# Kernel optimization log

Hardware: AMD Instinct MI355X
Metric: run time of the kernel (lower is better)

The kernel has to match this reference:

```python
import jax, jax.numpy as jnp
import numpy as np

OUT, IN = 4096, 4096
NNZ = 838860  # 0.05 * OUT * IN
ALPHA = 1.0   # set_privacy(True)


def setup_inputs() -> dict:
    key = jax.random.key(0)
    k1, k2, k3, k4, k5, k6 = jax.random.split(key, 6)
    x = jax.random.normal(k1, (2, 2048, IN), dtype=jnp.float32)
    # packed uint4 pairs stored as bytes (kept in int32 per spec; values in [0,256))
    base_packed = jax.random.randint(k2, (OUT, IN // 2), 0, 256, dtype=jnp.int32)
    # per-row dequant scales (positive, small, like ceiling/7)
    scales = jax.random.uniform(k3, (OUT, 1), dtype=jnp.float32, minval=1e-3, maxval=5e-2)
    ortho_vals = jax.random.normal(k4, (NNZ,), dtype=jnp.float32) * 0.02
    ortho_rows = jax.random.randint(k5, (NNZ,), 0, OUT, dtype=jnp.int32)
    ortho_cols = jax.random.randint(k6, (NNZ,), 0, IN, dtype=jnp.int32)
    return {"x": x, "base_packed": base_packed, "scales": scales,
            "ortho_vals": ortho_vals, "ortho_rows": ortho_rows, "ortho_cols": ortho_cols}


def _dequant(base_packed, scales):
    # unpack two int4 values per byte: col 2k <- low nibble, col 2k+1 <- high nibble
    p = base_packed.astype(jnp.int32)
    low = p & 0xF
    high = (p >> 4) & 0xF
    O, K = p.shape
    w_int4 = jnp.stack([low, high], axis=-1).reshape(O, 2 * K) - 8  # offset-binary -> [-8, 7]
    return w_int4.astype(jnp.float32) * scales  # [O, I]


def reference(x, base_packed, scales, ortho_vals, ortho_rows, ortho_cols):
    O = base_packed.shape[0]
    I = 2 * base_packed.shape[1]
    w_base = _dequant(base_packed, scales)  # [O, I] fp32
    # sparse outlier residual scattered into dense weight (CSR spmm equivalent)
    w_corr = jnp.zeros((O, I), jnp.float32).at[ortho_rows, ortho_cols].add(ortho_vals)
    w = w_base + ALPHA * w_corr
    x_flat = x.reshape(-1, I).astype(jnp.float32)
    out = x_flat @ w.T  # [N, O]
    return out.reshape(x.shape[:-1] + (O,)).astype(x.dtype)
```

## Files before the change

### kernel.cpp

```cpp
#include <hip/hip_runtime.h>
#include <cstdint>
#include <cstddef>

typedef __bf16 bf16x8 __attribute__((ext_vector_type(8)));
typedef float f32x4 __attribute__((ext_vector_type(4)));
typedef unsigned short ushort8 __attribute__((ext_vector_type(8)));

#define OUT_DIM 4096
#define IN_DIM 4096
#define NT 64


__device__ __forceinline__ unsigned short f2bf(float f) {
  unsigned u = __float_as_uint(f);
  return (unsigned short)((u + 0x7FFFu + ((u >> 16) & 1u)) >> 16);
}

__device__ __forceinline__ void async_copy16(const void* g, void* l) {
  __builtin_amdgcn_global_load_lds(
      (const __attribute__((address_space(1))) unsigned int*)g,
      (__attribute__((address_space(3))) unsigned int*)l, 16, 0, 0);
}


__global__ __launch_bounds__(256) void prep_kernel(
    const int* __restrict__ packed, const float* __restrict__ scales,
    unsigned short* __restrict__ wb, const float* __restrict__ x,
    unsigned short* __restrict__ xb) {
  int b = blockIdx.x;
  if (b < 8192) {
    int idx = b * 256 + threadIdx.x;
    int4 p = reinterpret_cast<const int4*>(packed)[idx];
    float s = scales[idx >> 9];
    ushort8 o;
    o[0] = f2bf((float)((p.x & 15) - 8) * s);
    o[1] = f2bf((float)(((p.x >> 4) & 15) - 8) * s);
    o[2] = f2bf((float)((p.y & 15) - 8) * s);
    o[3] = f2bf((float)(((p.y >> 4) & 15) - 8) * s);
    o[4] = f2bf((float)((p.z & 15) - 8) * s);
    o[5] = f2bf((float)(((p.z >> 4) & 15) - 8) * s);
    o[6] = f2bf((float)((p.w & 15) - 8) * s);
    o[7] = f2bf((float)(((p.w >> 4) & 15) - 8) * s);
    *reinterpret_cast<ushort8*>(&wb[(size_t)idx * 8]) = o;
  } else {
    int i = (b - 8192) * 256 + threadIdx.x;
    float4 a = reinterpret_cast<const float4*>(x)[2 * i];
    float4 c = reinterpret_cast<const float4*>(x)[2 * i + 1];
    ushort8 o;
    o[0] = f2bf(a.x); o[1] = f2bf(a.y); o[2] = f2bf(a.z); o[3] = f2bf(a.w);
    o[4] = f2bf(c.x); o[5] = f2bf(c.y); o[6] = f2bf(c.z); o[7] = f2bf(c.w);
    *reinterpret_cast<ushort8*>(&xb[(size_t)i * 8]) = o;
  }
}

__global__ __launch_bounds__(256) void scatter_pk_kernel(
    const float* __restrict__ vals, const int* __restrict__ rows,
    const int* __restrict__ cols, unsigned short* __restrict__ wb, int nnz) {
  int i = blockIdx.x * 256 + threadIdx.x;
  if (i >= nnz) return;
  size_t idx = (size_t)rows[i] * IN_DIM + cols[i];
  unsigned int* word = (unsigned int*)(wb + (idx & ~(size_t)1));
  unsigned short h = f2bf(vals[i]);
  unsigned int data = (idx & 1) ? ((unsigned)h << 16) : (unsigned)h;
  asm volatile("global_atomic_pk_add_bf16 %0, %1, off"
               :: "v"(word), "v"(data) : "memory");
}


#define SB(buf, op, kh) ((((buf) * 4) + ((op) * 2) + (kh)) * 16384)

#define STAGE(buf, op, kh, kt)                                              \
  do {                                                                      \
    const unsigned short* gsrc_ =                                           \
        (op) ? (const unsigned short*)((const char*)gA + dBA) : gA;         \
    const unsigned short* g_ = gsrc_ + (kt) * 64 + (kh) * 32;               \
    unsigned short* l_ =                                                    \
        (unsigned short*)((char*)lds + SB(buf, op, kh)) + wave * 512;       \
    async_copy16(g_, l_);                                                   \
    async_copy16(g_ + 128 * IN_DIM, l_ + 4096);                             \
  } while (0)

#define MFMA_ __builtin_amdgcn_mfma_f32_16x16x32_bf16

#define LDAQ(BUF, Q)                                                        \
  a00 = *(const bf16x8*)(ldsc + (laneA + SB(BUF, 0, 0) + (2*(Q)) * 1024));  \
  a01 = *(const bf16x8*)(ldsc + (laneA + SB(BUF, 0, 0) + (2*(Q)+1) * 1024));\
  a10 = *(const bf16x8*)(ldsc + (laneA + SB(BUF, 0, 1) + (2*(Q)) * 1024));  \
  a11 = *(const bf16x8*)(ldsc + (laneA + SB(BUF, 0, 1) + (2*(Q)+1) * 1024))

#define LDB4(d0, d1, d2, d3, BUF, KS)                                       \
  d0 = *(const bf16x8*)(ldsc + (laneB + SB(BUF, 1, KS) + 0));               \
  d1 = *(const bf16x8*)(ldsc + (laneB + SB(BUF, 1, KS) + 1024));            \
  d2 = *(const bf16x8*)(ldsc + (laneB + SB(BUF, 1, KS) + 2048));            \
  d3 = *(const bf16x8*)(ldsc + (laneB + SB(BUF, 1, KS) + 3072))

#define MMQ(Q)                                                              \
  acc[2*(Q)+0][0] = MFMA_(a00, b00, acc[2*(Q)+0][0], 0, 0, 0);              \
  acc[2*(Q)+0][1] = MFMA_(a00, b01, acc[2*(Q)+0][1], 0, 0, 0);              \
  acc[2*(Q)+0][2] = MFMA_(a00, b02, acc[2*(Q)+0][2], 0, 0, 0);              \
  acc[2*(Q)+0][3] = MFMA_(a00, b03, acc[2*(Q)+0][3], 0, 0, 0);              \
  acc[2*(Q)+1][0] = MFMA_(a01, b00, acc[2*(Q)+1][0], 0, 0, 0);              \
  acc[2*(Q)+1][1] = MFMA_(a01, b01, acc[2*(Q)+1][1], 0, 0, 0);              \
  acc[2*(Q)+1][2] = MFMA_(a01, b02, acc[2*(Q)+1][2], 0, 0, 0);              \
  acc[2*(Q)+1][3] = MFMA_(a01, b03, acc[2*(Q)+1][3], 0, 0, 0);              \
  acc[2*(Q)+0][0] = MFMA_(a10, b10, acc[2*(Q)+0][0], 0, 0, 0);              \
  acc[2*(Q)+0][1] = MFMA_(a10, b11, acc[2*(Q)+0][1], 0, 0, 0);              \
  acc[2*(Q)+0][2] = MFMA_(a10, b12, acc[2*(Q)+0][2], 0, 0, 0);              \
  acc[2*(Q)+0][3] = MFMA_(a10, b13, acc[2*(Q)+0][3], 0, 0, 0);              \
  acc[2*(Q)+1][0] = MFMA_(a11, b10, acc[2*(Q)+1][0], 0, 0, 0);              \
  acc[2*(Q)+1][1] = MFMA_(a11, b11, acc[2*(Q)+1][1], 0, 0, 0);              \
  acc[2*(Q)+1][2] = MFMA_(a11, b12, acc[2*(Q)+1][2], 0, 0, 0);              \
  acc[2*(Q)+1][3] = MFMA_(a11, b13, acc[2*(Q)+1][3], 0, 0, 0)

#define PH1(BUF, tS)                                                        \
  do {                                                                      \
    STAGE(1 - (BUF), 1, 0, tS);                                             \
    asm volatile("s_waitcnt vmcnt(2)" ::: "memory");                        \
    __builtin_amdgcn_s_barrier();                                           \
    LDB4(b00, b01, b02, b03, BUF, 0);                                       \
    LDB4(b10, b11, b12, b13, BUF, 1);                                       \
    LDAQ(BUF, 0);                                                           \
    asm volatile("s_waitcnt lgkmcnt(0)" ::: "memory");                      \
    __builtin_amdgcn_s_setprio(1);                                          \
    MMQ(0);                                                                 \
    __builtin_amdgcn_s_setprio(0);                                          \
    __builtin_amdgcn_s_barrier();                                           \
  } while (0)

#define PHQ(BUF, Q, OP, KH, tS)                                             \
  do {                                                                      \
    LDAQ(BUF, Q);                                                           \
    STAGE(1 - (BUF), OP, KH, tS);                                           \
    __builtin_amdgcn_s_barrier();                                           \
    asm volatile("s_waitcnt lgkmcnt(0)" ::: "memory");                      \
    __builtin_amdgcn_s_setprio(1);                                          \
    MMQ(Q);                                                                 \
    __builtin_amdgcn_s_setprio(0);                                          \
    __builtin_amdgcn_s_barrier();                                           \
  } while (0)

#define MINC(x) ((x) < NT ? (x) : (NT - 1))

#define TILE(BUF, t)                                                        \
  do {                                                                      \
    PH1(BUF, MINC((t) + 1));                                                \
    PHQ(BUF, 1, 1, 1, MINC((t) + 1));                                       \
    PHQ(BUF, 2, 0, 0, MINC((t) + 1));                                       \
    PHQ(BUF, 3, 0, 1, MINC((t) + 1));                                       \
  } while (0)

__global__ __launch_bounds__(512, 2) void gemm_kernel(
    const unsigned short* __restrict__ A,
    const unsigned short* __restrict__ B,
    float* __restrict__ C) {
  __shared__ __align__(16) unsigned short lds[65536];
  const char* ldsc = (const char*)lds;

  const int bid = blockIdx.x;
  const int xcd = bid & 7, i_ = bid >> 3;
  const int bm = (xcd >> 1) * 4 + (i_ >> 3);
  const int bn = (xcd & 1) * 8 + (i_ & 7);
  const int m0 = bm * 256, n0 = bn * 256;

  const int tid = threadIdx.x;
  const int wave = tid >> 6, lane = tid & 63;
  const int wm = wave >> 2, wn = wave & 3;
  const int lrow = lane & 15, lk = lane >> 4;

  const int r0 = tid >> 2, s0 = tid & 3;
  const int s0s = s0 ^ ((r0 >> 1) & 3);
  const unsigned short* gA = A + (size_t)(m0 + r0) * IN_DIM + s0s * 8;
  const ptrdiff_t dBA = ((const char*)B - (const char*)A) +
                        (ptrdiff_t)(n0 - m0) * IN_DIM * 2;

  const int lks = lk ^ ((lrow >> 1) & 3);
  const int laneA = (wm * 128 + lrow) * 64 + lks * 16;
  const int laneB = (wn * 64 + lrow) * 64 + lks * 16;

  f32x4 acc[8][4];
#pragma unroll
  for (int mi = 0; mi < 8; ++mi)
#pragma unroll
    for (int ni = 0; ni < 4; ++ni) acc[mi][ni] = (f32x4){0.f, 0.f, 0.f, 0.f};

  bf16x8 b00, b01, b02, b03, b10, b11, b12, b13;
  bf16x8 a00, a01, a10, a11;

  STAGE(0, 1, 0, 0);
  asm volatile("" ::: "memory");
  STAGE(0, 1, 1, 0);
  asm volatile("" ::: "memory");
  STAGE(0, 0, 0, 0);
  asm volatile("" ::: "memory");
  STAGE(0, 0, 1, 0);

#pragma unroll 1
  for (int p = 0; p < NT / 2; ++p) {
    TILE(0, 2 * p);
    TILE(1, 2 * p + 1);
  }
  asm volatile("s_waitcnt vmcnt(0) lgkmcnt(0)" ::: "memory");

#pragma unroll
  for (int mi = 0; mi < 8; ++mi)
#pragma unroll
    for (int ni = 0; ni < 4; ++ni) {
      int m = m0 + wm * 128 + mi * 16 + lk * 4;
      int n = n0 + wn * 64 + ni * 16 + lrow;
      float* cp = &C[(size_t)m * OUT_DIM + n];
#pragma unroll
      for (int r = 0; r < 4; ++r) cp[(size_t)r * OUT_DIM] = acc[mi][ni][r];
    }
}


extern "C" void kernel_launch(void* const* d_in, const int* in_sizes, int n_in,
                              void* d_out, int out_size, void* d_ws, size_t ws_size,
                              hipStream_t stream) {
  const float* x      = (const float*)d_in[0];
  const int*   packed = (const int*)d_in[1];
  const float* scales = (const float*)d_in[2];
  const float* vals   = (const float*)d_in[3];
  const int*   rows   = (const int*)d_in[4];
  const int*   cols   = (const int*)d_in[5];
  float* out = (float*)d_out;

  const int nnz = in_sizes[3];

  char* ws = (char*)d_ws;
  const size_t MB = 1024 * 1024;
  unsigned short* Wb = (unsigned short*)ws;
  unsigned short* Xb = (unsigned short*)(ws + 32 * MB);

  prep_kernel<<<16384, 256, 0, stream>>>(packed, scales, Wb, x, Xb);
  scatter_pk_kernel<<<(nnz + 255) / 256, 256, 0, stream>>>(vals, rows, cols, Wb, nnz);
  gemm_kernel<<<256, 512, 0, stream>>>(Xb, Wb, out);
}
```

Before: 182.7 us.

## Restructure GEMM main loop: two-tile prefetch and double-buffered A fragment loads

```diff
diff --git a/kernel.cpp b/kernel.cpp
--- a/kernel.cpp
+++ b/kernel.cpp
@@ -82,72 +82,74 @@
 
 #define MFMA_ __builtin_amdgcn_mfma_f32_16x16x32_bf16
 
-#define LDAQ(BUF, Q)                                                        \
-  a00 = *(const bf16x8*)(ldsc + (laneA + SB(BUF, 0, 0) + (2*(Q)) * 1024));  \
-  a01 = *(const bf16x8*)(ldsc + (laneA + SB(BUF, 0, 0) + (2*(Q)+1) * 1024));\
-  a10 = *(const bf16x8*)(ldsc + (laneA + SB(BUF, 0, 1) + (2*(Q)) * 1024));  \
-  a11 = *(const bf16x8*)(ldsc + (laneA + SB(BUF, 0, 1) + (2*(Q)+1) * 1024))
-
 #define LDB4(d0, d1, d2, d3, BUF, KS)                                       \
   d0 = *(const bf16x8*)(ldsc + (laneB + SB(BUF, 1, KS) + 0));               \
   d1 = *(const bf16x8*)(ldsc + (laneB + SB(BUF, 1, KS) + 1024));            \
   d2 = *(const bf16x8*)(ldsc + (laneB + SB(BUF, 1, KS) + 2048));            \
   d3 = *(const bf16x8*)(ldsc + (laneB + SB(BUF, 1, KS) + 3072))
 
-#define MMQ(Q)                                                              \
-  acc[2*(Q)+0][0] = MFMA_(a00, b00, acc[2*(Q)+0][0], 0, 0, 0);              \
-  acc[2*(Q)+0][1] = MFMA_(a00, b01, acc[2*(Q)+0][1], 0, 0, 0);              \
-  acc[2*(Q)+0][2] = MFMA_(a00, b02, acc[2*(Q)+0][2], 0, 0, 0);              \
-  acc[2*(Q)+0][3] = MFMA_(a00, b03, acc[2*(Q)+0][3], 0, 0, 0);              \
-  acc[2*(Q)+1][0] = MFMA_(a01, b00, acc[2*(Q)+1][0], 0, 0, 0);              \
-  acc[2*(Q)+1][1] = MFMA_(a01, b01, acc[2*(Q)+1][1], 0, 0, 0);              \
-  acc[2*(Q)+1][2] = MFMA_(a01, b02, acc[2*(Q)+1][2], 0, 0, 0);              \
-  acc[2*(Q)+1][3] = MFMA_(a01, b03, acc[2*(Q)+1][3], 0, 0, 0);              \
-  acc[2*(Q)+0][0] = MFMA_(a10, b10, acc[2*(Q)+0][0], 0, 0, 0);              \
-  acc[2*(Q)+0][1] = MFMA_(a10, b11, acc[2*(Q)+0][1], 0, 0, 0);              \
-  acc[2*(Q)+0][2] = MFMA_(a10, b12, acc[2*(Q)+0][2], 0, 0, 0);              \
-  acc[2*(Q)+0][3] = MFMA_(a10, b13, acc[2*(Q)+0][3], 0, 0, 0);              \
-  acc[2*(Q)+1][0] = MFMA_(a11, b10, acc[2*(Q)+1][0], 0, 0, 0);              \
-  acc[2*(Q)+1][1] = MFMA_(a11, b11, acc[2*(Q)+1][1], 0, 0, 0);              \
-  acc[2*(Q)+1][2] = MFMA_(a11, b12, acc[2*(Q)+1][2], 0, 0, 0);              \
-  acc[2*(Q)+1][3] = MFMA_(a11, b13, acc[2*(Q)+1][3], 0, 0, 0)
-
-#define PH1(BUF, tS)                                                        \
+#define LDAQ(R00, R01, R10, R11, BUF, Q)                                    \
+  R00 = *(const bf16x8*)(ldsc + (laneA + SB(BUF, 0, 0) + (2*(Q)) * 1024));  \
+  R01 = *(const bf16x8*)(ldsc + (laneA + SB(BUF, 0, 0) + (2*(Q)+1) * 1024));\
+  R10 = *(const bf16x8*)(ldsc + (laneA + SB(BUF, 0, 1) + (2*(Q)) * 1024));  \
+  R11 = *(const bf16x8*)(ldsc + (laneA + SB(BUF, 0, 1) + (2*(Q)+1) * 1024))
+
+#define MMQA(Q, A00, A01, A10, A11)                                         \
+  acc[2*(Q)+0][0] = MFMA_(A00, b00, acc[2*(Q)+0][0], 0, 0, 0);              \
+  acc[2*(Q)+0][1] = MFMA_(A00, b01, acc[2*(Q)+0][1], 0, 0, 0);              \
+  acc[2*(Q)+0][2] = MFMA_(A00, b02, acc[2*(Q)+0][2], 0, 0, 0);              \
+  acc[2*(Q)+0][3] = MFMA_(A00, b03, acc[2*(Q)+0][3], 0, 0, 0);              \
+  acc[2*(Q)+1][0] = MFMA_(A01, b00, acc[2*(Q)+1][0], 0, 0, 0);              \
+  acc[2*(Q)+1][1] = MFMA_(A01, b01, acc[2*(Q)+1][1], 0, 0, 0);              \
+  acc[2*(Q)+1][2] = MFMA_(A01, b02, acc[2*(Q)+1][2], 0, 0, 0);              \
+  acc[2*(Q)+1][3] = MFMA_(A01, b03, acc[2*(Q)+1][3], 0, 0, 0);              \
+  acc[2*(Q)+0][0] = MFMA_(A10, b10, acc[2*(Q)+0][0], 0, 0, 0);              \
+  acc[2*(Q)+0][1] = MFMA_(A10, b11, acc[2*(Q)+0][1], 0, 0, 0);              \
+  acc[2*(Q)+0][2] = MFMA_(A10, b12, acc[2*(Q)+0][2], 0, 0, 0);              \
+  acc[2*(Q)+0][3] = MFMA_(A10, b13, acc[2*(Q)+0][3], 0, 0, 0);              \
+  acc[2*(Q)+1][0] = MFMA_(A11, b10, acc[2*(Q)+1][0], 0, 0, 0);              \
+  acc[2*(Q)+1][1] = MFMA_(A11, b11, acc[2*(Q)+1][1], 0, 0, 0);              \
+  acc[2*(Q)+1][2] = MFMA_(A11, b12, acc[2*(Q)+1][2], 0, 0, 0);              \
+  acc[2*(Q)+1][3] = MFMA_(A11, b13, acc[2*(Q)+1][3], 0, 0, 0)
+
+#define SGB __builtin_amdgcn_sched_barrier(0)
+#define LGKM(N) asm volatile("s_waitcnt lgkmcnt(" #N ")" ::: "memory")
+
+#define TILE1(BUF, tS)                                                      \
   do {                                                                      \
-    STAGE(1 - (BUF), 1, 0, tS);                                             \
-    asm volatile("s_waitcnt vmcnt(2)" ::: "memory");                        \
+    asm volatile("s_waitcnt vmcnt(8)" ::: "memory");                        \
     __builtin_amdgcn_s_barrier();                                           \
     LDB4(b00, b01, b02, b03, BUF, 0);                                       \
     LDB4(b10, b11, b12, b13, BUF, 1);                                       \
-    LDAQ(BUF, 0);                                                           \
-    asm volatile("s_waitcnt lgkmcnt(0)" ::: "memory");                      \
-    __builtin_amdgcn_s_setprio(1);                                          \
-    MMQ(0);                                                                 \
+    LDAQ(aX00, aX01, aX10, aX11, BUF, 0);                                   \
+    SGB;                                    \
+    LDAQ(aY00, aY01, aY10, aY11, BUF, 1);                                   \
+    SGB; LGKM(4); SGB;                                                      \
+    __builtin_amdgcn_s_setprio(1);                                          \
+    MMQA(0, aX00, aX01, aX10, aX11);                                        \
+    __builtin_amdgcn_s_setprio(0);                                          \
+    SGB;                                                                    \
+    LDAQ(aX00, aX01, aX10, aX11, BUF, 2);                                   \
+    SGB; LGKM(4); SGB;                                                      \
+    __builtin_amdgcn_s_setprio(1);                                          \
+    MMQA(1, aY00, aY01, aY10, aY11);                                        \
+    __builtin_amdgcn_s_setprio(0);                                          \
+    SGB;                                                                    \
+    LDAQ(aY00, aY01, aY10, aY11, BUF, 3);                                   \
+    SGB; LGKM(4); SGB;                                                      \
+    __builtin_amdgcn_s_setprio(1);                                          \
+    MMQA(2, aX00, aX01, aX10, aX11);                                        \
+    __builtin_amdgcn_s_setprio(0);                                          \
+    SGB; LGKM(0); SGB;                                                      \
+    __builtin_amdgcn_s_setprio(1);                                          \
+    MMQA(3, aY00, aY01, aY10, aY11);                                        \
     __builtin_amdgcn_s_setprio(0);                                          \
     __builtin_amdgcn_s_barrier();                                           \
+    STAGE(BUF, 1, 0, tS); STAGE(BUF, 1, 1, tS);                             \
+    STAGE(BUF, 0, 0, tS); STAGE(BUF, 0, 1, tS);                             \
   } while (0)
 
-#define PHQ(BUF, Q, OP, KH, tS)                                             \
-  do {                                                                      \
-    LDAQ(BUF, Q);                                                           \
-    STAGE(1 - (BUF), OP, KH, tS);                                           \
-    __builtin_amdgcn_s_barrier();                                           \
-    asm volatile("s_waitcnt lgkmcnt(0)" ::: "memory");                      \
-    __builtin_amdgcn_s_setprio(1);                                          \
-    MMQ(Q);                                                                 \
-    __builtin_amdgcn_s_setprio(0);                                          \
-    __builtin_amdgcn_s_barrier();                                           \
-  } while (0)
-
 #define MINC(x) ((x) < NT ? (x) : (NT - 1))
-
-#define TILE(BUF, t)                                                        \
-  do {                                                                      \
-    PH1(BUF, MINC((t) + 1));                                                \
-    PHQ(BUF, 1, 1, 1, MINC((t) + 1));                                       \
-    PHQ(BUF, 2, 0, 0, MINC((t) + 1));                                       \
-    PHQ(BUF, 3, 0, 1, MINC((t) + 1));                                       \
-  } while (0)
 
 __global__ __launch_bounds__(512, 2) void gemm_kernel(
     const unsigned short* __restrict__ A,
@@ -184,20 +186,17 @@
     for (int ni = 0; ni < 4; ++ni) acc[mi][ni] = (f32x4){0.f, 0.f, 0.f, 0.f};
 
   bf16x8 b00, b01, b02, b03, b10, b11, b12, b13;
-  bf16x8 a00, a01, a10, a11;
-
-  STAGE(0, 1, 0, 0);
+  bf16x8 aX00, aX01, aX10, aX11;
+  bf16x8 aY00, aY01, aY10, aY11;
+
+  STAGE(0, 1, 0, 0); STAGE(0, 1, 1, 0); STAGE(0, 0, 0, 0); STAGE(0, 0, 1, 0);
   asm volatile("" ::: "memory");
-  STAGE(0, 1, 1, 0);
-  asm volatile("" ::: "memory");
-  STAGE(0, 0, 0, 0);
-  asm volatile("" ::: "memory");
-  STAGE(0, 0, 1, 0);
+  STAGE(1, 1, 0, 1); STAGE(1, 1, 1, 1); STAGE(1, 0, 0, 1); STAGE(1, 0, 1, 1);
 
 #pragma unroll 1
   for (int p = 0; p < NT / 2; ++p) {
-    TILE(0, 2 * p);
-    TILE(1, 2 * p + 1);
+    TILE1(0, MINC(2 * p + 2));
+    TILE1(1, MINC(2 * p + 3));
   }
   asm volatile("s_waitcnt vmcnt(0) lgkmcnt(0)" ::: "memory");
 
```

Result: slower. 196.2 us (+7.4%).

## Shrink GEMM tile to 128x256 with K=32 steps for higher occupancy

Applied to the files above, without the earlier changes.

```diff
diff --git a/kernel.cpp b/kernel.cpp
--- a/kernel.cpp
+++ b/kernel.cpp
@@ -8,7 +8,7 @@
 
 #define OUT_DIM 4096
 #define IN_DIM 4096
-#define NT 64
+#define NT 128
 
 
 __device__ __forceinline__ unsigned short f2bf(float f) {
@@ -67,100 +67,82 @@
 }
 
 
-#define SB(buf, op, kh) ((((buf) * 4) + ((op) * 2) + (kh)) * 16384)
-
-#define STAGE(buf, op, kh, kt)                                              \
+#define SBA(buf) ((buf) * 24576)
+#define SBB(buf) ((buf) * 24576 + 8192)
+
+#define STAGE_A(buf, kt)                                                    \
+  async_copy16(gA + (kt) * 32,                                              \
+               (char*)lds + SBA(buf) + wave * 1024)
+
+#define STAGE_B(buf, kt)                                                    \
   do {                                                                      \
-    const unsigned short* gsrc_ =                                           \
-        (op) ? (const unsigned short*)((const char*)gA + dBA) : gA;         \
-    const unsigned short* g_ = gsrc_ + (kt) * 64 + (kh) * 32;               \
-    unsigned short* l_ =                                                    \
-        (unsigned short*)((char*)lds + SB(buf, op, kh)) + wave * 512;       \
+    const unsigned short* g_ = gB + (kt) * 32;                              \
+    char* l_ = (char*)lds + SBB(buf) + wave * 1024;                         \
     async_copy16(g_, l_);                                                   \
-    async_copy16(g_ + 128 * IN_DIM, l_ + 4096);                             \
+    async_copy16(g_ + 128 * IN_DIM, l_ + 8192);                             \
   } while (0)
 
 #define MFMA_ __builtin_amdgcn_mfma_f32_16x16x32_bf16
 
-#define LDAQ(BUF, Q)                                                        \
-  a00 = *(const bf16x8*)(ldsc + (laneA + SB(BUF, 0, 0) + (2*(Q)) * 1024));  \
-  a01 = *(const bf16x8*)(ldsc + (laneA + SB(BUF, 0, 0) + (2*(Q)+1) * 1024));\
-  a10 = *(const bf16x8*)(ldsc + (laneA + SB(BUF, 0, 1) + (2*(Q)) * 1024));  \
-  a11 = *(const bf16x8*)(ldsc + (laneA + SB(BUF, 0, 1) + (2*(Q)+1) * 1024))
-
-#define LDB4(d0, d1, d2, d3, BUF, KS)                                       \
-  d0 = *(const bf16x8*)(ldsc + (laneB + SB(BUF, 1, KS) + 0));               \
-  d1 = *(const bf16x8*)(ldsc + (laneB + SB(BUF, 1, KS) + 1024));            \
-  d2 = *(const bf16x8*)(ldsc + (laneB + SB(BUF, 1, KS) + 2048));            \
-  d3 = *(const bf16x8*)(ldsc + (laneB + SB(BUF, 1, KS) + 3072))
-
-#define MMQ(Q)                                                              \
-  acc[2*(Q)+0][0] = MFMA_(a00, b00, acc[2*(Q)+0][0], 0, 0, 0);              \
-  acc[2*(Q)+0][1] = MFMA_(a00, b01, acc[2*(Q)+0][1], 0, 0, 0);              \
-  acc[2*(Q)+0][2] = MFMA_(a00, b02, acc[2*(Q)+0][2], 0, 0, 0);              \
-  acc[2*(Q)+0][3] = MFMA_(a00, b03, acc[2*(Q)+0][3], 0, 0, 0);              \
-  acc[2*(Q)+1][0] = MFMA_(a01, b00, acc[2*(Q)+1][0], 0, 0, 0);              \
-  acc[2*(Q)+1][1] = MFMA_(a01, b01, acc[2*(Q)+1][1], 0, 0, 0);              \
-  acc[2*(Q)+1][2] = MFMA_(a01, b02, acc[2*(Q)+1][2], 0, 0, 0);              \
-  acc[2*(Q)+1][3] = MFMA_(a01, b03, acc[2*(Q)+1][3], 0, 0, 0);              \
-  acc[2*(Q)+0][0] = MFMA_(a10, b10, acc[2*(Q)+0][0], 0, 0, 0);              \
-  acc[2*(Q)+0][1] = MFMA_(a10, b11, acc[2*(Q)+0][1], 0, 0, 0);              \
-  acc[2*(Q)+0][2] = MFMA_(a10, b12, acc[2*(Q)+0][2], 0, 0, 0);              \
-  acc[2*(Q)+0][3] = MFMA_(a10, b13, acc[2*(Q)+0][3], 0, 0, 0);              \
-  acc[2*(Q)+1][0] = MFMA_(a11, b10, acc[2*(Q)+1][0], 0, 0, 0);              \
-  acc[2*(Q)+1][1] = MFMA_(a11, b11, acc[2*(Q)+1][1], 0, 0, 0);              \
-  acc[2*(Q)+1][2] = MFMA_(a11, b12, acc[2*(Q)+1][2], 0, 0, 0);              \
-  acc[2*(Q)+1][3] = MFMA_(a11, b13, acc[2*(Q)+1][3], 0, 0, 0)
-
-#define PH1(BUF, tS)                                                        \
+#define LDA4(BUF)                                                           \
+  a0 = *(const bf16x8*)(ldsc + (laneA + SBA(BUF) + 0));                     \
+  a1 = *(const bf16x8*)(ldsc + (laneA + SBA(BUF) + 1024));                  \
+  a2 = *(const bf16x8*)(ldsc + (laneA + SBA(BUF) + 2048));                  \
+  a3 = *(const bf16x8*)(ldsc + (laneA + SBA(BUF) + 3072))
+
+#define LDB4(BUF)                                                           \
+  b0 = *(const bf16x8*)(ldsc + (laneB + SBB(BUF) + 0));                     \
+  b1 = *(const bf16x8*)(ldsc + (laneB + SBB(BUF) + 1024));                  \
+  b2 = *(const bf16x8*)(ldsc + (laneB + SBB(BUF) + 2048));                  \
+  b3 = *(const bf16x8*)(ldsc + (laneB + SBB(BUF) + 3072))
+
+#define MM16                                                                \
+  acc[0][0] = MFMA_(a0, b0, acc[0][0], 0, 0, 0);                            \
+  acc[0][1] = MFMA_(a0, b1, acc[0][1], 0, 0, 0);                            \
+  acc[0][2] = MFMA_(a0, b2, acc[0][2], 0, 0, 0);                            \
+  acc[0][3] = MFMA_(a0, b3, acc[0][3], 0, 0, 0);                            \
+  acc[1][0] = MFMA_(a1, b0, acc[1][0], 0, 0, 0);                            \
+  acc[1][1] = MFMA_(a1, b1, acc[1][1], 0, 0, 0);                            \
+  acc[1][2] = MFMA_(a1, b2, acc[1][2], 0, 0, 0);                            \
+  acc[1][3] = MFMA_(a1, b3, acc[1][3], 0, 0, 0);                            \
+  acc[2][0] = MFMA_(a2, b0, acc[2][0], 0, 0, 0);                            \
+  acc[2][1] = MFMA_(a2, b1, acc[2][1], 0, 0, 0);                            \
+  acc[2][2] = MFMA_(a2, b2, acc[2][2], 0, 0, 0);                            \
+  acc[2][3] = MFMA_(a2, b3, acc[2][3], 0, 0, 0);                            \
+  acc[3][0] = MFMA_(a3, b0, acc[3][0], 0, 0, 0);                            \
+  acc[3][1] = MFMA_(a3, b1, acc[3][1], 0, 0, 0);                            \
+  acc[3][2] = MFMA_(a3, b2, acc[3][2], 0, 0, 0);                            \
+  acc[3][3] = MFMA_(a3, b3, acc[3][3], 0, 0, 0)
+
+#define MINC(x) ((x) < NT ? (x) : (NT - 1))
+
+#define TILE(BUF, tS)                                                       \
   do {                                                                      \
-    STAGE(1 - (BUF), 1, 0, tS);                                             \
-    asm volatile("s_waitcnt vmcnt(2)" ::: "memory");                        \
+    STAGE_A(1 - (BUF), tS);                                                 \
+    STAGE_B(1 - (BUF), tS);                                                 \
+    asm volatile("s_waitcnt vmcnt(3)" ::: "memory");                        \
     __builtin_amdgcn_s_barrier();                                           \
-    LDB4(b00, b01, b02, b03, BUF, 0);                                       \
-    LDB4(b10, b11, b12, b13, BUF, 1);                                       \
-    LDAQ(BUF, 0);                                                           \
+    LDA4(BUF);                                                              \
+    LDB4(BUF);                                                              \
     asm volatile("s_waitcnt lgkmcnt(0)" ::: "memory");                      \
     __builtin_amdgcn_s_setprio(1);                                          \
-    MMQ(0);                                                                 \
+    MM16;                                                                   \
     __builtin_amdgcn_s_setprio(0);                                          \
     __builtin_amdgcn_s_barrier();                                           \
   } while (0)
 
-#define PHQ(BUF, Q, OP, KH, tS)                                             \
-  do {                                                                      \
-    LDAQ(BUF, Q);                                                           \
-    STAGE(1 - (BUF), OP, KH, tS);                                           \
-    __builtin_amdgcn_s_barrier();                                           \
-    asm volatile("s_waitcnt lgkmcnt(0)" ::: "memory");                      \
-    __builtin_amdgcn_s_setprio(1);                                          \
-    MMQ(Q);                                                                 \
-    __builtin_amdgcn_s_setprio(0);                                          \
-    __builtin_amdgcn_s_barrier();                                           \
-  } while (0)
-
-#define MINC(x) ((x) < NT ? (x) : (NT - 1))
-
-#define TILE(BUF, t)                                                        \
-  do {                                                                      \
-    PH1(BUF, MINC((t) + 1));                                                \
-    PHQ(BUF, 1, 1, 1, MINC((t) + 1));                                       \
-    PHQ(BUF, 2, 0, 0, MINC((t) + 1));                                       \
-    PHQ(BUF, 3, 0, 1, MINC((t) + 1));                                       \
-  } while (0)
-
-__global__ __launch_bounds__(512, 2) void gemm_kernel(
+__global__ __launch_bounds__(512, 4) void gemm_kernel(
     const unsigned short* __restrict__ A,
     const unsigned short* __restrict__ B,
     float* __restrict__ C) {
-  __shared__ __align__(16) unsigned short lds[65536];
+  __shared__ __align__(16) unsigned short lds[24576];
   const char* ldsc = (const char*)lds;
 
   const int bid = blockIdx.x;
   const int xcd = bid & 7, i_ = bid >> 3;
-  const int bm = (xcd >> 1) * 4 + (i_ >> 3);
+  const int bm = (xcd >> 1) * 8 + (i_ >> 3);
   const int bn = (xcd & 1) * 8 + (i_ & 7);
-  const int m0 = bm * 256, n0 = bn * 256;
+  const int m0 = bm * 128, n0 = bn * 256;
 
   const int tid = threadIdx.x;
   const int wave = tid >> 6, lane = tid & 63;
@@ -170,42 +152,35 @@
   const int r0 = tid >> 2, s0 = tid & 3;
   const int s0s = s0 ^ ((r0 >> 1) & 3);
   const unsigned short* gA = A + (size_t)(m0 + r0) * IN_DIM + s0s * 8;
-  const ptrdiff_t dBA = ((const char*)B - (const char*)A) +
-                        (ptrdiff_t)(n0 - m0) * IN_DIM * 2;
+  const unsigned short* gB = B + (size_t)(n0 + r0) * IN_DIM + s0s * 8;
 
   const int lks = lk ^ ((lrow >> 1) & 3);
-  const int laneA = (wm * 128 + lrow) * 64 + lks * 16;
+  const int laneA = (wm * 64 + lrow) * 64 + lks * 16;
   const int laneB = (wn * 64 + lrow) * 64 + lks * 16;
 
-  f32x4 acc[8][4];
-#pragma unroll
-  for (int mi = 0; mi < 8; ++mi)
+  f32x4 acc[4][4];
+#pragma unroll
+  for (int mi = 0; mi < 4; ++mi)
 #pragma unroll
     for (int ni = 0; ni < 4; ++ni) acc[mi][ni] = (f32x4){0.f, 0.f, 0.f, 0.f};
 
-  bf16x8 b00, b01, b02, b03, b10, b11, b12, b13;
-  bf16x8 a00, a01, a10, a11;
-
-  STAGE(0, 1, 0, 0);
-  asm volatile("" ::: "memory");
-  STAGE(0, 1, 1, 0);
-  asm volatile("" ::: "memory");
-  STAGE(0, 0, 0, 0);
-  asm volatile("" ::: "memory");
-  STAGE(0, 0, 1, 0);
+  bf16x8 a0, a1, a2, a3, b0, b1, b2, b3;
+
+  STAGE_A(0, 0);
+  STAGE_B(0, 0);
 
 #pragma unroll 1
   for (int p = 0; p < NT / 2; ++p) {
-    TILE(0, 2 * p);
-    TILE(1, 2 * p + 1);
+    TILE(0, MINC(2 * p + 1));
+    TILE(1, MINC(2 * p + 2));
   }
   asm volatile("s_waitcnt vmcnt(0) lgkmcnt(0)" ::: "memory");
 
 #pragma unroll
-  for (int mi = 0; mi < 8; ++mi)
+  for (int mi = 0; mi < 4; ++mi)
 #pragma unroll
     for (int ni = 0; ni < 4; ++ni) {
-      int m = m0 + wm * 128 + mi * 16 + lk * 4;
+      int m = m0 + wm * 64 + mi * 16 + lk * 4;
       int n = n0 + wn * 64 + ni * 16 + lrow;
       float* cp = &C[(size_t)m * OUT_DIM + n];
 #pragma unroll
@@ -234,5 +209,5 @@
 
   prep_kernel<<<16384, 256, 0, stream>>>(packed, scales, Wb, x, Xb);
   scatter_pk_kernel<<<(nnz + 255) / 256, 256, 0, stream>>>(vals, rows, cols, Wb, nnz);
-  gemm_kernel<<<256, 512, 0, stream>>>(Xb, Wb, out);
-}
+  gemm_kernel<<<512, 512, 0, stream>>>(Xb, Wb, out);
+}
```

Result: slower. 202.9 us (+11.1%).
